# Optimization experiments

Hardware: AMD Instinct MI355X
Metric: run time of the kernel (lower is better)

The kernel has to match this reference:

```python
import jax, jax.numpy as jnp
import numpy as np
from jax import lax

LN_EPS = 1e-5

def _conv1d(h, w, b):
    # h: [N, L, Cin], w: [Cout, Cin, K] (torch Conv1d layout), padding=1
    out = lax.conv_general_dilated(h, w, window_strides=(1,), padding=[(1, 1)],
                                   dimension_numbers=("NWC", "OIW", "NWC"))
    return out + b

def _layer_norm(h, g, b):
    m = jnp.mean(h, axis=-1, keepdims=True)
    v = jnp.mean((h - m) ** 2, axis=-1, keepdims=True)
    return (h - m) * lax.rsqrt(v + LN_EPS) * g + b

def setup_inputs() -> dict:
    key = jax.random.key(0)
    ks = jax.random.split(key, 8)
    N, L, D, F = 32, 512, 384, 256
    return {
        "x": jax.random.normal(ks[0], (N, L, D), jnp.float32),
        "conv1_w": jax.random.normal(ks[1], (F, D, 3), jnp.float32) * 0.05,
        "conv1_b": jnp.zeros((F,), jnp.float32),
        "ln1_g": jnp.ones((F,), jnp.float32),
        "ln1_b": jnp.zeros((F,), jnp.float32),
        "conv2_w": jax.random.normal(ks[2], (F, F, 3), jnp.float32) * 0.05,
        "conv2_b": jnp.zeros((F,), jnp.float32),
        "ln2_g": jnp.ones((F,), jnp.float32),
        "ln2_b": jnp.zeros((F,), jnp.float32),
        "lin_w": jax.random.normal(ks[3], (F,), jnp.float32) * 0.05,
        "lin_b": jnp.zeros((), jnp.float32),
        "target": jax.random.randint(ks[4], (N, L), 0, 8, dtype=jnp.int32),
        "mel_max_length": 2048,
    }

def reference(x, conv1_w, conv1_b, ln1_g, ln1_b, conv2_w, conv2_b, ln2_g, ln2_b,
              lin_w, lin_b, target, mel_max_length):
    # Duration predictor (dropout is identity at inference)
    h = jax.nn.relu(_layer_norm(_conv1d(x, conv1_w, conv1_b), ln1_g, ln1_b))
    h = jax.nn.relu(_layer_norm(_conv1d(h, conv2_w, conv2_b), ln2_g, ln2_b))
    duration_predictor_output = jnp.einsum("nlf,f->nl", h, lin_w) + lin_b  # [N, L]

    # LR: frame t copies phoneme j iff cumsum(dur)[:j] <= t < cumsum(dur)[:j+1]
    # (equivalent to the one-hot alignment matmul, padded to mel_max_length)
    N, L, D = x.shape
    T = mel_max_length
    cums = jnp.cumsum(target, axis=-1)                      # [N, L]
    frames = jnp.arange(T, dtype=cums.dtype)                # [T]
    idx = jax.vmap(lambda c: jnp.searchsorted(c, frames, side="right"))(cums)  # [N, T]
    valid = frames[None, :] < cums[:, -1:]                  # frames beyond total are zero
    gathered = jnp.take_along_axis(x, jnp.clip(idx, 0, L - 1)[:, :, None], axis=1)
    output = gathered * valid[:, :, None].astype(x.dtype)   # [N, T, D]
    return output, duration_predictor_output
```

## Files before the change

### kernel.cpp

```cpp
#include <hip/hip_runtime.h>
#include <hip/hip_bf16.h>

#define NB   32
#define TMEL 2048

typedef unsigned short u16;
typedef short s8v __attribute__((ext_vector_type(8)));
typedef float f4v __attribute__((ext_vector_type(4)));
typedef u16 u16x8 __attribute__((ext_vector_type(8)));

static __device__ __forceinline__ u16 f2bf(float v) {
    __hip_bfloat16 h = __float2bfloat16(v);
    return *(u16*)&h;
}

__global__ __launch_bounds__(256) void prep_kernel(
    const float* __restrict__ w1,
    const float* __restrict__ w2,
    const int*   __restrict__ target,
    u16* __restrict__ Wt1,
    u16* __restrict__ Wt2,
    int* __restrict__ idxv,
    u16* __restrict__ zbuf)
{
    __shared__ int c[512];
    const int b = blockIdx.x, tid = threadIdx.x;
    if (b == 0 && tid < 8) {
        u16x8 z = {0, 0, 0, 0, 0, 0, 0, 0};
        *(u16x8*)(zbuf + tid * 8) = z;
    }
    if (b < 1152) {
        const int K = 1152, DIN = 384;
        int e = b * 256 + tid;
        int f = e / K;
        int rem = e - f * K;
        int kc = rem / DIN;
        int d = rem - kc * DIN;
        Wt1[e] = f2bf(w1[f * K + d * 3 + kc]);
    } else if (b < 1920) {
        const int K = 768, DIN = 256;
        int e = (b - 1152) * 256 + tid;
        int f = e / K;
        int rem = e - f * K;
        int kc = rem / DIN;
        int d = rem - kc * DIN;
        Wt2[e] = f2bf(w2[f * K + d * 3 + kc]);
    } else {
        const int n = b - 1920;
        c[tid]       = target[n * 512 + tid];
        c[tid + 256] = target[n * 512 + 256 + tid];
        __syncthreads();
        for (int off = 1; off < 512; off <<= 1) {
            int v0 = (tid       >= off) ? c[tid       - off] : 0;
            int v1 = (tid + 256 >= off) ? c[tid + 256 - off] : 0;
            __syncthreads();
            c[tid]       += v0;
            c[tid + 256] += v1;
            __syncthreads();
        }
        const int total = c[511];
        for (int t = tid; t < TMEL; t += 256) {
            int lo = 0, hi = 512;
            while (lo < hi) {
                int mid = (lo + hi) >> 1;
                if (c[mid] <= t) lo = mid + 1; else hi = mid;
            }
            idxv[n * TMEL + t] = (t < total) ? min(lo, 511) : -1;
        }
    }
}

template<int DIN, int MODE, int ASRC>
__global__ __launch_bounds__(256, 2) void conv_mfma_kernel(
    const void* __restrict__ Ainp,
    const u16* __restrict__ Wt,
    const float* __restrict__ cb,
    const float* __restrict__ g,
    const float* __restrict__ bb,
    const float* __restrict__ lw,
    const float* __restrict__ lbp,
    const u16* __restrict__ zbuf,
    void* __restrict__ outp)
{
    const int K = 3 * DIN, NT = K / 64;
    __shared__ __align__(128) char AsB[2][32 * 128];
    __shared__ __align__(128) char BsB[2][256 * 128];
    __shared__ float redS[32 * 4];
    __shared__ float redQ[32 * 4];
    __shared__ float redP[32 * 4];

    const int tid  = threadIdx.x;
    const int lane = tid & 63, wc = tid >> 6;
    const int lr = lane & 15, q4 = lane >> 4;
    const int sb = (blockIdx.x & 7) * 64 + (blockIdx.x >> 3);
    const int m0 = sb * 32;
    const int n  = m0 >> 9, l0 = m0 & 511;

    f4v acc[2][4];
    #pragma unroll
    for (int mi = 0; mi < 2; mi++)
        #pragma unroll
        for (int ni = 0; ni < 4; ni++) acc[mi][ni] = {0.f, 0.f, 0.f, 0.f};

    const int a_r    = tid >> 3;
    const int a_slot = (tid & 7) ^ (a_r & 7);
    const int b_r    = tid >> 3;
    const int b_slot = (tid & 7) ^ (b_r & 7);

    const int aoff0 = (lr) * 128;
    const int aoff1 = (16 + lr) * 128;
    int boff[4];
    #pragma unroll
    for (int ni = 0; ni < 4; ni++) boff[ni] = (64 * wc + 16 * ni + lr) * 128;
    const int slot0 = ((q4)     ^ (lr & 7)) << 4;
    const int slot1 = ((q4 | 4) ^ (lr & 7)) << 4;

    auto stage = [&](int buf, int t) {
        const int k0 = t * 64;
        const int kc = k0 / DIN;
        const int d0 = k0 - kc * DIN;
        const int lp = l0 + a_r + kc - 1;
        if (ASRC == 0) {
            f4v v0 = {0.f, 0.f, 0.f, 0.f}, v1 = v0;
            if (lp >= 0 && lp < 512) {
                const float* src = (const float*)Ainp
                    + ((size_t)((n << 9) + lp)) * DIN + d0 + (tid & 7) * 8;
                v0 = *(const f4v*)src;
                v1 = *(const f4v*)(src + 4);
            }
            u16x8 r;
            #pragma unroll
            for (int jj = 0; jj < 4; jj++) { r[jj] = f2bf(v0[jj]); r[4 + jj] = f2bf(v1[jj]); }
            *(u16x8*)(AsB[buf] + a_r * 128 + a_slot * 16) = r;
        } else {
            const u16* asrc = (lp >= 0 && lp < 512)
                ? ((const u16*)Ainp + ((size_t)((n << 9) + lp)) * DIN + d0 + a_slot * 8)
                : zbuf;
            __builtin_amdgcn_global_load_lds(
                (const __attribute__((address_space(1))) void*)asrc,
                (__attribute__((address_space(3))) void*)(AsB[buf] + tid * 16), 16, 0, 0);
        }
        const u16* bsrc = Wt + (size_t)b_r * K + k0 + b_slot * 8;
        #pragma unroll
        for (int q = 0; q < 8; q++) {
            __builtin_amdgcn_global_load_lds(
                (const __attribute__((address_space(1))) void*)(bsrc + (size_t)q * 32 * K),
                (__attribute__((address_space(3))) void*)(BsB[buf] + q * 4096 + tid * 16),
                16, 0, 0);
        }
    };

    auto compute = [&](int buf) {
        #pragma unroll
        for (int kk = 0; kk < 2; kk++) {
            const int sl = kk ? slot1 : slot0;
            s8v a0 = *(const s8v*)(AsB[buf] + aoff0 + sl);
            s8v a1 = *(const s8v*)(AsB[buf] + aoff1 + sl);
            s8v b0 = *(const s8v*)(BsB[buf] + boff[0] + sl);
            s8v b1 = *(const s8v*)(BsB[buf] + boff[1] + sl);
            s8v b2 = *(const s8v*)(BsB[buf] + boff[2] + sl);
            s8v b3 = *(const s8v*)(BsB[buf] + boff[3] + sl);
            acc[0][0] = __builtin_amdgcn_mfma_f32_16x16x32_bf16(a0, b0, acc[0][0], 0, 0, 0);
            acc[0][1] = __builtin_amdgcn_mfma_f32_16x16x32_bf16(a0, b1, acc[0][1], 0, 0, 0);
            acc[0][2] = __builtin_amdgcn_mfma_f32_16x16x32_bf16(a0, b2, acc[0][2], 0, 0, 0);
            acc[0][3] = __builtin_amdgcn_mfma_f32_16x16x32_bf16(a0, b3, acc[0][3], 0, 0, 0);
            acc[1][0] = __builtin_amdgcn_mfma_f32_16x16x32_bf16(a1, b0, acc[1][0], 0, 0, 0);
            acc[1][1] = __builtin_amdgcn_mfma_f32_16x16x32_bf16(a1, b1, acc[1][1], 0, 0, 0);
            acc[1][2] = __builtin_amdgcn_mfma_f32_16x16x32_bf16(a1, b2, acc[1][2], 0, 0, 0);
            acc[1][3] = __builtin_amdgcn_mfma_f32_16x16x32_bf16(a1, b3, acc[1][3], 0, 0, 0);
        }
    };

    stage(0, 0);
    __syncthreads();
    int cur = 0;
    for (int t = 0; t < NT; ++t) {
        if (t + 1 < NT) stage(cur ^ 1, t + 1);
        compute(cur);
        __syncthreads();
        cur ^= 1;
    }

    float cbv[4], gv[4], bbv[4], lwv[4];
    int col[4];
    #pragma unroll
    for (int ni = 0; ni < 4; ni++) {
        col[ni] = 64 * wc + 16 * ni + lr;
        cbv[ni] = cb[col[ni]]; gv[ni] = g[col[ni]]; bbv[ni] = bb[col[ni]];
        if (MODE == 1) lwv[ni] = lw[col[ni]];
    }

    float sv[2][4], sq[2][4];
    #pragma unroll
    for (int mi = 0; mi < 2; mi++)
        #pragma unroll
        for (int reg = 0; reg < 4; reg++) {
            float s = 0.f, q = 0.f;
            #pragma unroll
            for (int ni = 0; ni < 4; ni++) {
                float v = acc[mi][ni][reg] + cbv[ni];
                s += v; q += v * v;
            }
            #pragma unroll
            for (int msk = 1; msk < 16; msk <<= 1) {
                s += __shfl_xor(s, msk);
                q += __shfl_xor(q, msk);
            }
            sv[mi][reg] = s; sq[mi][reg] = q;
        }
    if (lr == 0) {
        #pragma unroll
        for (int mi = 0; mi < 2; mi++)
            #pragma unroll
            for (int reg = 0; reg < 4; reg++) {
                int rl = 16 * mi + 4 * q4 + reg;
                redS[rl * 4 + wc] = sv[mi][reg];
                redQ[rl * 4 + wc] = sq[mi][reg];
            }
    }
    __syncthreads();

    float mean_[2][4], rs_[2][4];
    #pragma unroll
    for (int mi = 0; mi < 2; mi++)
        #pragma unroll
        for (int reg = 0; reg < 4; reg++) {
            int rl = 16 * mi + 4 * q4 + reg;
            float4 ps = *(float4*)&redS[rl * 4];
            float4 pq = *(float4*)&redQ[rl * 4];
            float mean = (ps.x + ps.y + ps.z + ps.w) * (1.f / 256.f);
            float var  = (pq.x + pq.y + pq.z + pq.w) * (1.f / 256.f) - mean * mean;
            mean_[mi][reg] = mean;
            rs_[mi][reg]   = rsqrtf(var + 1e-5f);
        }

    if (MODE == 0) {
        u16* hout = (u16*)outp;
        #pragma unroll
        for (int mi = 0; mi < 2; mi++)
            #pragma unroll
            for (int reg = 0; reg < 4; reg++) {
                int rl = 16 * mi + 4 * q4 + reg;
                #pragma unroll
                for (int ni = 0; ni < 4; ni++) {
                    float v = acc[mi][ni][reg] + cbv[ni];
                    float o = fmaxf(0.f, (v - mean_[mi][reg]) * rs_[mi][reg] * gv[ni] + bbv[ni]);
                    hout[(size_t)(m0 + rl) * 256 + col[ni]] = f2bf(o);
                }
            }
    } else {
        float pp[2][4];
        #pragma unroll
        for (int mi = 0; mi < 2; mi++)
            #pragma unroll
            for (int reg = 0; reg < 4; reg++) {
                float p = 0.f;
                #pragma unroll
                for (int ni = 0; ni < 4; ni++) {
                    float v = acc[mi][ni][reg] + cbv[ni];
                    float o = fmaxf(0.f, (v - mean_[mi][reg]) * rs_[mi][reg] * gv[ni] + bbv[ni]);
                    p += o * lwv[ni];
                }
                #pragma unroll
                for (int msk = 1; msk < 16; msk <<= 1) p += __shfl_xor(p, msk);
                pp[mi][reg] = p;
            }
        if (lr == 0) {
            #pragma unroll
            for (int mi = 0; mi < 2; mi++)
                #pragma unroll
                for (int reg = 0; reg < 4; reg++) {
                    int rl = 16 * mi + 4 * q4 + reg;
                    redP[rl * 4 + wc] = pp[mi][reg];
                }
        }
        __syncthreads();
        if (tid < 32) {
            float* dpo = (float*)outp;
            float4 p4 = *(float4*)&redP[tid * 4];
            dpo[m0 + tid] = p4.x + p4.y + p4.z + p4.w + lbp[0];
        }
    }
}

__global__ void lr_gather_kernel(const float* __restrict__ x,
                                 const int* __restrict__ idxv,
                                 float* __restrict__ out) {
    int gid = blockIdx.x * 256 + threadIdx.x;
    int f4  = gid % 48;
    int row = gid / 48;
    int n   = row >> 11;
    int ie  = idxv[row];
    f4v v0 = {0.f, 0.f, 0.f, 0.f}, v1 = v0;
    if (ie >= 0) {
        const float* src = &x[((size_t)(n << 9) + ie) * 384];
        v0 = *(const f4v*)&src[f4 * 4];
        v1 = *(const f4v*)&src[(f4 + 48) * 4];
    }
    float* dst = &out[(size_t)row * 384];
    __builtin_nontemporal_store(v0, (f4v*)&dst[f4 * 4]);
    __builtin_nontemporal_store(v1, (f4v*)&dst[(f4 + 48) * 4]);
}

extern "C" void kernel_launch(void* const* d_in, const int* in_sizes, int n_in,
                              void* d_out, int out_size, void* d_ws, size_t ws_size,
                              hipStream_t stream) {
    const float* x   = (const float*)d_in[0];
    const float* w1  = (const float*)d_in[1];
    const float* b1  = (const float*)d_in[2];
    const float* g1  = (const float*)d_in[3];
    const float* bb1 = (const float*)d_in[4];
    const float* w2  = (const float*)d_in[5];
    const float* b2  = (const float*)d_in[6];
    const float* g2  = (const float*)d_in[7];
    const float* bb2 = (const float*)d_in[8];
    const float* lw  = (const float*)d_in[9];
    const float* lb  = (const float*)d_in[10];
    const int* target = (const int*)d_in[11];

    char* wsb  = (char*)d_ws;
    u16*  zbuf = (u16*)wsb;
    u16*  Wt1  = (u16*)(wsb + 128);
    u16*  Wt2  = (u16*)(wsb + 128 + 589824);
    u16*  h1   = (u16*)(wsb + 128 + 589824 + 393216);
    int*  idxv = (int*)(wsb + 128 + 589824 + 393216 + 8388608);

    float* out0 = (float*)d_out;
    float* dpo  = out0 + (size_t)32 * 2048 * 384;

    prep_kernel<<<1952, 256, 0, stream>>>(w1, w2, target, Wt1, Wt2, idxv, zbuf);

    conv_mfma_kernel<384, 0, 0><<<512, 256, 0, stream>>>(
        (const void*)x, Wt1, b1, g1, bb1, nullptr, nullptr, zbuf, (void*)h1);
    conv_mfma_kernel<256, 1, 1><<<512, 256, 0, stream>>>(
        (const void*)h1, Wt2, b2, g2, bb2, lw, lb, zbuf, (void*)dpo);

    lr_gather_kernel<<<12288, 256, 0, stream>>>(x, idxv, out0);
}
```

Baseline: 78.89 us.

## Fuse prep, both convs and gather into one cooperative persistent kernel

Replaces four separate launches (weight transpose/scan prep, two conv+LN kernels, LR gather) with a single cooperative kernel of 512 blocks that uses grid-wide syncs between phases. The intent is to remove launch gaps and kernel-boundary drain/fill overhead. The gather phase now runs with only 512 blocks looping over the output, which may lower memory-level parallelism for the dominant store-bound part. Grid syncs add their own cost, and co-residency requires that all 512 blocks fit on the device at once.

```diff
diff --git a/kernel.cpp b/kernel.cpp
--- a/kernel.cpp
+++ b/kernel.cpp
@@ -1,5 +1,6 @@
 #include <hip/hip_runtime.h>
 #include <hip/hip_bf16.h>
+#include <hip/hip_cooperative_groups.h>
 
 #define NB   32
 #define TMEL 2048
@@ -14,81 +15,16 @@
     return *(u16*)&h;
 }
 
-__global__ __launch_bounds__(256) void prep_kernel(
-    const float* __restrict__ w1,
-    const float* __restrict__ w2,
-    const int*   __restrict__ target,
-    u16* __restrict__ Wt1,
-    u16* __restrict__ Wt2,
-    int* __restrict__ idxv,
-    u16* __restrict__ zbuf)
-{
-    __shared__ int c[512];
-    const int b = blockIdx.x, tid = threadIdx.x;
-    if (b == 0 && tid < 8) {
-        u16x8 z = {0, 0, 0, 0, 0, 0, 0, 0};
-        *(u16x8*)(zbuf + tid * 8) = z;
-    }
-    if (b < 1152) {
-        const int K = 1152, DIN = 384;
-        int e = b * 256 + tid;
-        int f = e / K;
-        int rem = e - f * K;
-        int kc = rem / DIN;
-        int d = rem - kc * DIN;
-        Wt1[e] = f2bf(w1[f * K + d * 3 + kc]);
-    } else if (b < 1920) {
-        const int K = 768, DIN = 256;
-        int e = (b - 1152) * 256 + tid;
-        int f = e / K;
-        int rem = e - f * K;
-        int kc = rem / DIN;
-        int d = rem - kc * DIN;
-        Wt2[e] = f2bf(w2[f * K + d * 3 + kc]);
-    } else {
-        const int n = b - 1920;
-        c[tid]       = target[n * 512 + tid];
-        c[tid + 256] = target[n * 512 + 256 + tid];
-        __syncthreads();
-        for (int off = 1; off < 512; off <<= 1) {
-            int v0 = (tid       >= off) ? c[tid       - off] : 0;
-            int v1 = (tid + 256 >= off) ? c[tid + 256 - off] : 0;
-            __syncthreads();
-            c[tid]       += v0;
-            c[tid + 256] += v1;
-            __syncthreads();
-        }
-        const int total = c[511];
-        for (int t = tid; t < TMEL; t += 256) {
-            int lo = 0, hi = 512;
-            while (lo < hi) {
-                int mid = (lo + hi) >> 1;
-                if (c[mid] <= t) lo = mid + 1; else hi = mid;
-            }
-            idxv[n * TMEL + t] = (t < total) ? min(lo, 511) : -1;
-        }
-    }
-}
-
 template<int DIN, int MODE, int ASRC>
-__global__ __launch_bounds__(256, 2) void conv_mfma_kernel(
-    const void* __restrict__ Ainp,
-    const u16* __restrict__ Wt,
-    const float* __restrict__ cb,
-    const float* __restrict__ g,
-    const float* __restrict__ bb,
-    const float* __restrict__ lw,
-    const float* __restrict__ lbp,
-    const u16* __restrict__ zbuf,
-    void* __restrict__ outp)
+static __device__ __forceinline__ void conv_phase(
+    const void* __restrict__ Ainp, const u16* __restrict__ Wt,
+    const float* __restrict__ cb, const float* __restrict__ g,
+    const float* __restrict__ bb, const float* __restrict__ lw,
+    const float* __restrict__ lbp, const u16* __restrict__ zbuf,
+    void* __restrict__ outp,
+    char* AsB0, char* BsB0, float* redS, float* redQ, float* redP)
 {
     const int K = 3 * DIN, NT = K / 64;
-    __shared__ __align__(128) char AsB[2][32 * 128];
-    __shared__ __align__(128) char BsB[2][256 * 128];
-    __shared__ float redS[32 * 4];
-    __shared__ float redQ[32 * 4];
-    __shared__ float redP[32 * 4];
-
     const int tid  = threadIdx.x;
     const int lane = tid & 63, wc = tid >> 6;
     const int lr = lane & 15, q4 = lane >> 4;
@@ -116,6 +52,8 @@
     const int slot1 = ((q4 | 4) ^ (lr & 7)) << 4;
 
     auto stage = [&](int buf, int t) {
+        char* AsB = AsB0 + buf * 4096;
+        char* BsB = BsB0 + buf * 32768;
         const int k0 = t * 64;
         const int kc = k0 / DIN;
         const int d0 = k0 - kc * DIN;
@@ -131,35 +69,37 @@
             u16x8 r;
             #pragma unroll
             for (int jj = 0; jj < 4; jj++) { r[jj] = f2bf(v0[jj]); r[4 + jj] = f2bf(v1[jj]); }
-            *(u16x8*)(AsB[buf] + a_r * 128 + a_slot * 16) = r;
+            *(u16x8*)(AsB + a_r * 128 + a_slot * 16) = r;
         } else {
             const u16* asrc = (lp >= 0 && lp < 512)
                 ? ((const u16*)Ainp + ((size_t)((n << 9) + lp)) * DIN + d0 + a_slot * 8)
                 : zbuf;
             __builtin_amdgcn_global_load_lds(
                 (const __attribute__((address_space(1))) void*)asrc,
-                (__attribute__((address_space(3))) void*)(AsB[buf] + tid * 16), 16, 0, 0);
+                (__attribute__((address_space(3))) void*)(AsB + tid * 16), 16, 0, 0);
         }
         const u16* bsrc = Wt + (size_t)b_r * K + k0 + b_slot * 8;
         #pragma unroll
         for (int q = 0; q < 8; q++) {
             __builtin_amdgcn_global_load_lds(
                 (const __attribute__((address_space(1))) void*)(bsrc + (size_t)q * 32 * K),
-                (__attribute__((address_space(3))) void*)(BsB[buf] + q * 4096 + tid * 16),
+                (__attribute__((address_space(3))) void*)(BsB + q * 4096 + tid * 16),
                 16, 0, 0);
         }
     };
 
     auto compute = [&](int buf) {
+        char* AsB = AsB0 + buf * 4096;
+        char* BsB = BsB0 + buf * 32768;
         #pragma unroll
         for (int kk = 0; kk < 2; kk++) {
             const int sl = kk ? slot1 : slot0;
-            s8v a0 = *(const s8v*)(AsB[buf] + aoff0 + sl);
-            s8v a1 = *(const s8v*)(AsB[buf] + aoff1 + sl);
-            s8v b0 = *(const s8v*)(BsB[buf] + boff[0] + sl);
-            s8v b1 = *(const s8v*)(BsB[buf] + boff[1] + sl);
-            s8v b2 = *(const s8v*)(BsB[buf] + boff[2] + sl);
-            s8v b3 = *(const s8v*)(BsB[buf] + boff[3] + sl);
+            s8v a0 = *(const s8v*)(AsB + aoff0 + sl);
+            s8v a1 = *(const s8v*)(AsB + aoff1 + sl);
+            s8v b0 = *(const s8v*)(BsB + boff[0] + sl);
+            s8v b1 = *(const s8v*)(BsB + boff[1] + sl);
+            s8v b2 = *(const s8v*)(BsB + boff[2] + sl);
+            s8v b3 = *(const s8v*)(BsB + boff[3] + sl);
             acc[0][0] = __builtin_amdgcn_mfma_f32_16x16x32_bf16(a0, b0, acc[0][0], 0, 0, 0);
             acc[0][1] = __builtin_amdgcn_mfma_f32_16x16x32_bf16(a0, b1, acc[0][1], 0, 0, 0);
             acc[0][2] = __builtin_amdgcn_mfma_f32_16x16x32_bf16(a0, b2, acc[0][2], 0, 0, 0);
@@ -283,23 +223,101 @@
     }
 }
 
-__global__ void lr_gather_kernel(const float* __restrict__ x,
-                                 const int* __restrict__ idxv,
-                                 float* __restrict__ out) {
-    int gid = blockIdx.x * 256 + threadIdx.x;
-    int f4  = gid % 48;
-    int row = gid / 48;
-    int n   = row >> 11;
-    int ie  = idxv[row];
-    f4v v0 = {0.f, 0.f, 0.f, 0.f}, v1 = v0;
-    if (ie >= 0) {
-        const float* src = &x[((size_t)(n << 9) + ie) * 384];
-        v0 = *(const f4v*)&src[f4 * 4];
-        v1 = *(const f4v*)&src[(f4 + 48) * 4];
-    }
-    float* dst = &out[(size_t)row * 384];
-    __builtin_nontemporal_store(v0, (f4v*)&dst[f4 * 4]);
-    __builtin_nontemporal_store(v1, (f4v*)&dst[(f4 + 48) * 4]);
+__global__ __launch_bounds__(256, 2) void mega_kernel(
+    const float* __restrict__ x,
+    const float* __restrict__ w1, const float* __restrict__ w2,
+    const int* __restrict__ target,
+    const float* __restrict__ cb1, const float* __restrict__ g1,
+    const float* __restrict__ bb1,
+    const float* __restrict__ cb2, const float* __restrict__ g2,
+    const float* __restrict__ bb2,
+    const float* __restrict__ lw, const float* __restrict__ lbp,
+    u16* __restrict__ Wt1, u16* __restrict__ Wt2,
+    u16* __restrict__ h1, int* __restrict__ idxv, u16* __restrict__ zbuf,
+    float* __restrict__ out0, float* __restrict__ dpo)
+{
+    __shared__ __align__(128) char AsB0[2 * 32 * 128];
+    __shared__ __align__(128) char BsB0[2 * 256 * 128];
+    __shared__ float redS[32 * 4];
+    __shared__ float redQ[32 * 4];
+    __shared__ float redP[32 * 4];
+
+    cooperative_groups::grid_group grid = cooperative_groups::this_grid();
+    const int tid  = threadIdx.x;
+    const int b    = blockIdx.x;
+    const int gtid = b * 256 + tid;
+
+    if (gtid < 8) {
+        u16x8 z = {0, 0, 0, 0, 0, 0, 0, 0};
+        *(u16x8*)(zbuf + gtid * 8) = z;
+    }
+    for (int e = gtid; e < 294912; e += 131072) {
+        int f = e / 1152;
+        int rem = e - f * 1152;
+        int kc = rem / 384;
+        int d = rem - kc * 384;
+        Wt1[e] = f2bf(w1[f * 1152 + d * 3 + kc]);
+    }
+    for (int e = gtid; e < 196608; e += 131072) {
+        int f = e / 768;
+        int rem = e - f * 768;
+        int kc = rem / 256;
+        int d = rem - kc * 256;
+        Wt2[e] = f2bf(w2[f * 768 + d * 3 + kc]);
+    }
+    if (b < 64) {
+        const int n = b >> 1, half = b & 1;
+        int* c = (int*)AsB0;
+        c[tid]       = target[n * 512 + tid];
+        c[tid + 256] = target[n * 512 + 256 + tid];
+        __syncthreads();
+        for (int off = 1; off < 512; off <<= 1) {
+            int v0 = (tid       >= off) ? c[tid       - off] : 0;
+            int v1 = (tid + 256 >= off) ? c[tid + 256 - off] : 0;
+            __syncthreads();
+            c[tid]       += v0;
+            c[tid + 256] += v1;
+            __syncthreads();
+        }
+        const int total = c[511];
+        for (int t = half * 1024 + tid; t < half * 1024 + 1024; t += 256) {
+            int lo = 0, hi = 512;
+            while (lo < hi) {
+                int mid = (lo + hi) >> 1;
+                if (c[mid] <= t) lo = mid + 1; else hi = mid;
+            }
+            idxv[n * TMEL + t] = (t < total) ? min(lo, 511) : -1;
+        }
+        __syncthreads();
+    }
+    __threadfence();
+    grid.sync();
+
+    conv_phase<384, 0, 0>((const void*)x, Wt1, cb1, g1, bb1, nullptr, nullptr,
+                          zbuf, (void*)h1, AsB0, BsB0, redS, redQ, redP);
+    __threadfence();
+    grid.sync();
+
+    conv_phase<256, 1, 1>((const void*)h1, Wt2, cb2, g2, bb2, lw, lbp,
+                          zbuf, (void*)dpo, AsB0, BsB0, redS, redQ, redP);
+
+    #pragma unroll 4
+    for (int it = 0; it < 24; ++it) {
+        int u   = gtid + it * 131072;
+        int j   = u % 48;
+        int row = u / 48;
+        int n   = row >> 11;
+        int ie  = idxv[row];
+        f4v v0 = {0.f, 0.f, 0.f, 0.f}, v1 = v0;
+        if (ie >= 0) {
+            const float* src = &x[((size_t)(n << 9) + ie) * 384];
+            v0 = *(const f4v*)&src[j * 4];
+            v1 = *(const f4v*)&src[(j + 48) * 4];
+        }
+        float* dst = &out0[(size_t)row * 384];
+        __builtin_nontemporal_store(v0, (f4v*)&dst[j * 4]);
+        __builtin_nontemporal_store(v1, (f4v*)&dst[(j + 48) * 4]);
+    }
 }
 
 extern "C" void kernel_launch(void* const* d_in, const int* in_sizes, int n_in,
@@ -328,12 +346,14 @@
     float* out0 = (float*)d_out;
     float* dpo  = out0 + (size_t)32 * 2048 * 384;
 
-    prep_kernel<<<1952, 256, 0, stream>>>(w1, w2, target, Wt1, Wt2, idxv, zbuf);
-
-    conv_mfma_kernel<384, 0, 0><<<512, 256, 0, stream>>>(
-        (const void*)x, Wt1, b1, g1, bb1, nullptr, nullptr, zbuf, (void*)h1);
-    conv_mfma_kernel<256, 1, 1><<<512, 256, 0, stream>>>(
-        (const void*)h1, Wt2, b2, g2, bb2, lw, lb, zbuf, (void*)dpo);
-
-    lr_gather_kernel<<<12288, 256, 0, stream>>>(x, idxv, out0);
+    void* args[] = {
+        (void*)&x, (void*)&w1, (void*)&w2, (void*)&target,
+        (void*)&b1, (void*)&g1, (void*)&bb1,
+        (void*)&b2, (void*)&g2, (void*)&bb2,
+        (void*)&lw, (void*)&lb,
+        (void*)&Wt1, (void*)&Wt2, (void*)&h1, (void*)&idxv, (void*)&zbuf,
+        (void*)&out0, (void*)&dpo
+    };
+    hipLaunchCooperativeKernel((void*)mega_kernel, dim3(512), dim3(256),
+                               args, 0, stream);
 }
```

Result: slower. 277.9 us (+252.3%).

## Fuse length-regulator gather into prep kernel and drop separate gather launch

Applied to the files above, without the earlier changes.

Merges the LR gather into the prep kernel. Each of 1024 blocks recomputes the cumsum for its batch, binary-searches 64 frames into shared memory, and writes those 64 output rows directly, while the remaining blocks convert the conv weights. This removes the idxv round trip through global memory and one kernel launch, and lets the large gather write overlap with weight preparation. In exchange, every block repeats the 512-element scan (32x redundant per batch).

```diff
diff --git a/kernel.cpp b/kernel.cpp
--- a/kernel.cpp
+++ b/kernel.cpp
@@ -14,59 +14,86 @@
     return *(u16*)&h;
 }
 
-__global__ __launch_bounds__(256) void prep_kernel(
+__global__ __launch_bounds__(256) void gather_prep_kernel(
+    const float* __restrict__ x,
+    const int*   __restrict__ target,
     const float* __restrict__ w1,
     const float* __restrict__ w2,
-    const int*   __restrict__ target,
     u16* __restrict__ Wt1,
     u16* __restrict__ Wt2,
-    int* __restrict__ idxv,
-    u16* __restrict__ zbuf)
+    u16* __restrict__ zbuf,
+    float* __restrict__ out0)
 {
     __shared__ int c[512];
+    __shared__ int ridx[64];
     const int b = blockIdx.x, tid = threadIdx.x;
-    if (b == 0 && tid < 8) {
-        u16x8 z = {0, 0, 0, 0, 0, 0, 0, 0};
-        *(u16x8*)(zbuf + tid * 8) = z;
-    }
-    if (b < 1152) {
-        const int K = 1152, DIN = 384;
-        int e = b * 256 + tid;
-        int f = e / K;
-        int rem = e - f * K;
-        int kc = rem / DIN;
-        int d = rem - kc * DIN;
-        Wt1[e] = f2bf(w1[f * K + d * 3 + kc]);
-    } else if (b < 1920) {
-        const int K = 768, DIN = 256;
-        int e = (b - 1152) * 256 + tid;
-        int f = e / K;
-        int rem = e - f * K;
-        int kc = rem / DIN;
-        int d = rem - kc * DIN;
-        Wt2[e] = f2bf(w2[f * K + d * 3 + kc]);
-    } else {
-        const int n = b - 1920;
-        c[tid]       = target[n * 512 + tid];
-        c[tid + 256] = target[n * 512 + 256 + tid];
+
+    if (b >= 1024) {
+        if (b == 1024 && tid < 8) {
+            u16x8 z = {0, 0, 0, 0, 0, 0, 0, 0};
+            *(u16x8*)(zbuf + tid * 8) = z;
+        }
+        if (b < 2176) {
+            const int K = 1152, DIN = 384;
+            int e = (b - 1024) * 256 + tid;
+            int f = e / K;
+            int rem = e - f * K;
+            int kc = rem / DIN;
+            int d = rem - kc * DIN;
+            Wt1[e] = f2bf(w1[f * K + d * 3 + kc]);
+        } else {
+            const int K = 768, DIN = 256;
+            int e = (b - 2176) * 256 + tid;
+            int f = e / K;
+            int rem = e - f * K;
+            int kc = rem / DIN;
+            int d = rem - kc * DIN;
+            Wt2[e] = f2bf(w2[f * K + d * 3 + kc]);
+        }
+        return;
+    }
+
+    const int n = b >> 5, sub = b & 31;
+    c[tid]       = target[n * 512 + tid];
+    c[tid + 256] = target[n * 512 + 256 + tid];
+    __syncthreads();
+    for (int off = 1; off < 512; off <<= 1) {
+        int v0 = (tid       >= off) ? c[tid       - off] : 0;
+        int v1 = (tid + 256 >= off) ? c[tid + 256 - off] : 0;
         __syncthreads();
-        for (int off = 1; off < 512; off <<= 1) {
-            int v0 = (tid       >= off) ? c[tid       - off] : 0;
-            int v1 = (tid + 256 >= off) ? c[tid + 256 - off] : 0;
-            __syncthreads();
-            c[tid]       += v0;
-            c[tid + 256] += v1;
-            __syncthreads();
-        }
-        const int total = c[511];
-        for (int t = tid; t < TMEL; t += 256) {
-            int lo = 0, hi = 512;
-            while (lo < hi) {
-                int mid = (lo + hi) >> 1;
-                if (c[mid] <= t) lo = mid + 1; else hi = mid;
-            }
-            idxv[n * TMEL + t] = (t < total) ? min(lo, 511) : -1;
-        }
+        c[tid]       += v0;
+        c[tid + 256] += v1;
+        __syncthreads();
+    }
+    const int total = c[511];
+    if (tid < 64) {
+        int t = sub * 64 + tid;
+        int lo = 0, hi = 512;
+        while (lo < hi) {
+            int mid = (lo + hi) >> 1;
+            if (c[mid] <= t) lo = mid + 1; else hi = mid;
+        }
+        ridx[tid] = (t < total) ? min(lo, 511) : -1;
+    }
+    __syncthreads();
+
+    const size_t xbase = (size_t)(n << 9) * 384;
+    const size_t obase = ((size_t)(n << 11) + sub * 64) * 384;
+    #pragma unroll 4
+    for (int it = 0; it < 12; ++it) {
+        int u  = tid + it * 256;
+        int j  = u % 48;
+        int rl = u / 48;
+        int ie = ridx[rl];
+        f4v v0 = {0.f, 0.f, 0.f, 0.f}, v1 = v0;
+        if (ie >= 0) {
+            const float* src = &x[xbase + (size_t)ie * 384];
+            v0 = *(const f4v*)&src[j * 4];
+            v1 = *(const f4v*)&src[(j + 48) * 4];
+        }
+        float* dst = &out0[obase + (size_t)rl * 384];
+        __builtin_nontemporal_store(v0, (f4v*)&dst[j * 4]);
+        __builtin_nontemporal_store(v1, (f4v*)&dst[(j + 48) * 4]);
     }
 }
 
@@ -283,25 +310,6 @@
     }
 }
 
-__global__ void lr_gather_kernel(const float* __restrict__ x,
-                                 const int* __restrict__ idxv,
-                                 float* __restrict__ out) {
-    int gid = blockIdx.x * 256 + threadIdx.x;
-    int f4  = gid % 48;
-    int row = gid / 48;
-    int n   = row >> 11;
-    int ie  = idxv[row];
-    f4v v0 = {0.f, 0.f, 0.f, 0.f}, v1 = v0;
-    if (ie >= 0) {
-        const float* src = &x[((size_t)(n << 9) + ie) * 384];
-        v0 = *(const f4v*)&src[f4 * 4];
-        v1 = *(const f4v*)&src[(f4 + 48) * 4];
-    }
-    float* dst = &out[(size_t)row * 384];
-    __builtin_nontemporal_store(v0, (f4v*)&dst[f4 * 4]);
-    __builtin_nontemporal_store(v1, (f4v*)&dst[(f4 + 48) * 4]);
-}
-
 extern "C" void kernel_launch(void* const* d_in, const int* in_sizes, int n_in,
                               void* d_out, int out_size, void* d_ws, size_t ws_size,
                               hipStream_t stream) {
@@ -323,17 +331,16 @@
     u16*  Wt1  = (u16*)(wsb + 128);
     u16*  Wt2  = (u16*)(wsb + 128 + 589824);
     u16*  h1   = (u16*)(wsb + 128 + 589824 + 393216);
-    int*  idxv = (int*)(wsb + 128 + 589824 + 393216 + 8388608);
 
     float* out0 = (float*)d_out;
     float* dpo  = out0 + (size_t)32 * 2048 * 384;
 
-    prep_kernel<<<1952, 256, 0, stream>>>(w1, w2, target, Wt1, Wt2, idxv, zbuf);
+    gather_prep_kernel<<<2944, 256, 0, stream>>>(
+        x, target, w1, w2, Wt1, Wt2, zbuf, out0);
 
     conv_mfma_kernel<384, 0, 0><<<512, 256, 0, stream>>>(
         (const void*)x, Wt1, b1, g1, bb1, nullptr, nullptr, zbuf, (void*)h1);
+
     conv_mfma_kernel<256, 1, 1><<<512, 256, 0, stream>>>(
         (const void*)h1, Wt2, b2, g2, bb2, lw, lb, zbuf, (void*)dpo);
-
-    lr_gather_kernel<<<12288, 256, 0, stream>>>(x, idxv, out0);
 }
```

Result: faster. 71.56 us (-9.3%).
